# Kernel optimization log

Measured on AMD Instinct MI355X. Metric: run time of the kernel, lower is better.

Reference implementation:

```python
import jax, jax.numpy as jnp
import numpy as np

EPS = 1e-4

def _mlp2(x, W1, b1, W2, b2):
    # Sequential(Linear, ReLU, Linear) -> [*, 1]
    return jax.nn.relu(x @ W1 + b1) @ W2 + b2

def setup_inputs() -> dict:
    N, D = 400, 64
    key = jax.random.key(0)
    ks = jax.random.split(key, 24)
    s = 0.1
    inp = {
        "t": 0,
        "node_edge_embedding": jax.random.normal(ks[0], (N + N * N, D), jnp.float32),
        "node_flow_norm": jax.random.normal(ks[1], (N, D), jnp.float32),
        "A_ne": jax.random.uniform(ks[2], (N, N * N), jnp.float32),
        "node_num": N,
        # alpha_n_dedunce
        "W_alpha": jax.random.normal(ks[3], (D, D), jnp.float32) * s,
        "b_alpha": jnp.zeros((D,), jnp.float32),
        # gamma_e_dedunce
        "W_gamma": jax.random.normal(ks[4], (D, D), jnp.float32) * s,
        "b_gamma": jnp.zeros((D,), jnp.float32),
        # node_to_edge (2D -> D)
        "W_n2e": jax.random.normal(ks[5], (2 * D, D), jnp.float32) * s,
        "b_n2e": jnp.zeros((D,), jnp.float32),
        # edge_to_value: D -> D//2 -> 1
        "W_ev1": jax.random.normal(ks[6], (D, D // 2), jnp.float32) * s,
        "b_ev1": jnp.zeros((D // 2,), jnp.float32),
        "W_ev2": jax.random.normal(ks[7], (D // 2, 1), jnp.float32) * s,
        "b_ev2": jnp.zeros((1,), jnp.float32),
        # f_theta: D -> D//2 -> 1
        "W_ft1": jax.random.normal(ks[8], (D, D // 2), jnp.float32) * s,
        "b_ft1": jnp.zeros((D // 2,), jnp.float32),
        "W_ft2": jax.random.normal(ks[9], (D // 2, 1), jnp.float32) * s,
        "b_ft2": jnp.zeros((1,), jnp.float32),
        # W_3, W_4 (init.normal_ std=0.1)
        "W3": jax.random.normal(ks[10], (D, D), jnp.float32) * s,
        "W4": jax.random.normal(ks[11], (D, D), jnp.float32) * s,
        # edge_to_edge
        "W_e2e": jax.random.normal(ks[12], (D, D), jnp.float32) * s,
        "b_e2e": jnp.zeros((D,), jnp.float32),
        # node_to_edge_2 (2D -> D)
        "W_n2e2": jax.random.normal(ks[13], (2 * D, D), jnp.float32) * s,
        "b_n2e2": jnp.zeros((D,), jnp.float32),
    }
    return inp

def reference(t, node_edge_embedding, node_flow_norm, A_ne, node_num,
              W_alpha, b_alpha, W_gamma, b_gamma, W_n2e, b_n2e,
              W_ev1, b_ev1, W_ev2, b_ev2, W_ft1, b_ft1, W_ft2, b_ft2,
              W3, W4, W_e2e, b_e2e, W_n2e2, b_n2e2):
    N = node_num
    D = node_flow_norm.shape[1]
    node_emb = node_edge_embedding[:N]          # [N, D]
    edge_emb = node_edge_embedding[N:]          # [N*N, D]

    # fully-connected cartesian edge features: edges[i*N+j] = [node_i, node_j]
    edges = jnp.concatenate(
        [jnp.broadcast_to(node_emb[:, None, :], (N, N, D)),
         jnp.broadcast_to(node_emb[None, :, :], (N, N, D))], axis=-1
    ).reshape(N * N, 2 * D)                     # [N*N, 2D]

    h = edges @ W_n2e + b_n2e                   # node_to_edge
    A = jax.nn.relu(_mlp2(h, W_ev1, b_ev1, W_ev2, b_ev2)).reshape(N, N)

    # degree normalization: D_mat A D_mat with D_mat = diag(1/sqrt(clamp(rowsum)))
    d = 1.0 / jnp.sqrt(jnp.maximum(jnp.sum(A, axis=1), EPS))  # [N]
    normalized_A = d[:, None] * A * d[None, :]

    massage_conv = (normalized_A @ node_emb) @ W3
    alpha_n = massage_conv @ W_alpha + b_alpha
    alpha_n = alpha_n / jnp.maximum(jnp.max(jnp.abs(alpha_n)), EPS)

    denominator = _mlp2(node_flow_norm, W_ft1, b_ft1, W_ft2, b_ft2)   # [N,1]
    norm_value = _mlp2(node_emb, W_ft1, b_ft1, W_ft2, b_ft2) / \
        jnp.where(denominator == 0, EPS, denominator)
    node_self_evolve = norm_value * (jax.nn.relu(node_flow_norm - node_emb) @ W4)
    node_self_evolve = alpha_n * node_self_evolve

    gamma_e = jax.nn.softmax(edge_emb @ W_gamma + b_gamma, axis=1)    # [N*N, D]
    edge_indicator = jnp.where(A < 1.0, 0.0, 1.0).reshape(-1, 1)      # [N*N, 1]
    Aggr_edge = A_ne @ (edge_indicator * gamma_e * edge_emb)          # [N, D]
    pred_node = node_self_evolve + Aggr_edge

    edge_self_evolve = edge_emb @ W_e2e + b_e2e
    edge_infonode = edges @ W_n2e2 + b_n2e2
    pred_edge = edge_indicator * (edge_self_evolve + edge_infonode)

    pred_node_edge = jnp.concatenate([pred_node, pred_edge], axis=0)
    return pred_node_edge, edge_indicator
```

## Files before the change

kernel.cpp:

```cpp
#include <hip/hip_runtime.h>

#define NV_N 400
#define NN   160000
#define EPSV 1e-4f
#define IND_BASE ((size_t)160400 * 64)

#define OFF_A    0
#define OFF_P2   160000
#define OFF_Q2   172800
#define OFF_R    185600
#define OFF_S    211200
#define OFF_V4   236800
#define OFF_AR   262400
#define OFF_NV   288000
#define OFF_DV   288400
#define OFF_GMAX 288800
#define OFF_CNT  288832
#define OFF_LIST 289280
#define OFF_WV   449280

__global__ __launch_bounds__(64) void k1_node_pre(
    const float* __restrict__ NEE, const float* __restrict__ NFN,
    const float* __restrict__ W_n2e, const float* __restrict__ b_n2e,
    const float* __restrict__ W_n2e2, const float* __restrict__ b_n2e2,
    const float* __restrict__ W_ev1, const float* __restrict__ b_ev1,
    const float* __restrict__ W4,
    const float* __restrict__ W_ft1, const float* __restrict__ b_ft1,
    const float* __restrict__ W_ft2, const float* __restrict__ b_ft2,
    float* __restrict__ ws)
{
    __shared__ float xne[64], xnf[64], tP[64], tQ[64], hidN[32], hidF[32];
    int i = blockIdx.x, dd = threadIdx.x;
    float x_ne = NEE[i*64+dd];
    float x_nf = NFN[i*64+dd];
    xne[dd] = x_ne; xnf[dd] = x_nf;
    if (i == 0 && dd == 0) ((unsigned*)(ws + OFF_GMAX))[0] = 0u;
    __syncthreads();
    float pv = b_n2e[dd], qv = 0.f, rv = b_n2e2[dd], sv = 0.f, v4 = 0.f;
    for (int k = 0; k < 64; ++k) {
        float xk = xne[k];
        pv += xk * W_n2e[k*64+dd];
        qv += xk * W_n2e[(64+k)*64+dd];
        rv += xk * W_n2e2[k*64+dd];
        sv += xk * W_n2e2[(64+k)*64+dd];
        v4 += fmaxf(xnf[k]-xk, 0.f) * W4[k*64+dd];
    }
    tP[dd] = pv; tQ[dd] = qv;
    ws[OFF_R  + i*64+dd] = rv;
    ws[OFF_S  + i*64+dd] = sv;
    ws[OFF_V4 + i*64+dd] = v4;
    if (dd < 32) {
        float hn = b_ft1[dd], hf = b_ft1[dd];
        for (int k = 0; k < 64; ++k) { hn += xne[k]*W_ft1[k*32+dd]; hf += xnf[k]*W_ft1[k*32+dd]; }
        hidN[dd] = fmaxf(hn, 0.f); hidF[dd] = fmaxf(hf, 0.f);
    }
    __syncthreads();
    if (dd < 32) {
        float p2 = b_ev1[dd], q2 = 0.f;
        for (int c = 0; c < 64; ++c) { p2 += tP[c]*W_ev1[c*32+dd]; q2 += tQ[c]*W_ev1[c*32+dd]; }
        ws[OFF_P2 + i*32+dd] = p2;
        ws[OFF_Q2 + i*32+dd] = q2;
    }
    if (dd == 0) {
        float num = b_ft2[0], den = b_ft2[0];
        for (int c = 0; c < 32; ++c) { num += hidN[c]*W_ft2[c]; den += hidF[c]*W_ft2[c]; }
        float dv = (den == 0.f) ? EPSV : den;
        ws[OFF_NV + i] = num / dv;
    }
}

__global__ __launch_bounds__(256) void k2_row(
    const float* __restrict__ NEE,
    const float* __restrict__ W_ev2, const float* __restrict__ b_ev2,
    const float* __restrict__ W_e2e, const float* __restrict__ b_e2e,
    float* __restrict__ ws, float* __restrict__ out)
{
    __shared__ float p2s[32], wev2[32], red[256];
    __shared__ int rcnt[256];
    __shared__ unsigned char flag[NV_N];
    __shared__ int act[NV_N];
    __shared__ int s_cnt;
    int i = blockIdx.x, t = threadIdx.x;
    if (t < 32) { p2s[t] = ws[OFF_P2 + i*32+t]; wev2[t] = W_ev2[t]; }
    __syncthreads();
    float b2 = b_ev2[0];
    float s = 0.f; int cc = 0;
    for (int j = t; j < NV_N; j += 256) {
        float v = b2;
        #pragma unroll
        for (int c = 0; c < 32; ++c) {
            float h = p2s[c] + ws[OFF_Q2 + j*32+c];
            v += fmaxf(h, 0.f) * wev2[c];
        }
        float a = fmaxf(v, 0.f);
        ws[OFF_A + i*NV_N + j] = a;
        bool f = (a >= 1.0f);
        flag[j] = f ? 1 : 0;
        out[IND_BASE + (size_t)i*NV_N + j] = f ? 1.f : 0.f;
        s += a; cc += f ? 1 : 0;
    }
    red[t] = s; rcnt[t] = cc;
    __syncthreads();
    for (int st = 128; st > 0; st >>= 1) {
        if (t < st) { red[t] += red[t+st]; rcnt[t] += rcnt[t+st]; }
        __syncthreads();
    }
    if (t == 0) {
        ws[OFF_DV + i] = rsqrtf(fmaxf(red[0], EPSV));
        ((int*)ws)[OFF_CNT + i] = rcnt[0];
    }
    if (t < 64) {
        int base = 0;
        for (int ch = 0; ch < 7; ++ch) {
            int j = ch*64 + t;
            bool f = (j < NV_N) && (flag[j] != 0);
            unsigned long long m = __ballot(f);
            if (f) {
                int pre = __popcll(m & ((1ull << t) - 1ull));
                act[base + pre] = j;
            }
            base += __popcll(m);
        }
        if (t == 0) s_cnt = base;
    }
    float4 z4 = make_float4(0.f, 0.f, 0.f, 0.f);
    float4* orow = (float4*)(out + (NV_N + (size_t)i*NV_N) * 64);
    for (int q = t; q < NV_N*64/4; q += 256) orow[q] = z4;
    __syncthreads();
    int cnt = s_cnt, lane = t & 63, w = t >> 6;
    for (int k = w; k < cnt; k += 4) {
        int j = act[k];
        int e = i*NV_N + j;
        float emb = NEE[(size_t)(NV_N + e)*64 + lane];
        float v = b_e2e[lane] + ws[OFF_R + i*64 + lane] + ws[OFF_S + j*64 + lane];
        #pragma unroll
        for (int c = 0; c < 64; ++c) v += __shfl(emb, c) * W_e2e[c*64 + lane];
        out[(size_t)(NV_N + e)*64 + lane] = v;
    }
}

__global__ __launch_bounds__(256) void k3_alpha_compact(
    const float* __restrict__ NEE,
    const float* __restrict__ W3,
    const float* __restrict__ W_alpha, const float* __restrict__ b_alpha,
    const float* __restrict__ W_gamma, const float* __restrict__ b_gamma,
    float* __restrict__ ws, int cap)
{
    __shared__ float part[4][64];
    __shared__ int red[256];
    __shared__ int s_off;
    int i = blockIdx.x, t = threadIdx.x, lane = t & 63, w = t >> 6;
    int os = 0;
    for (int r = t; r < i; r += 256) os += ((const int*)ws)[OFF_CNT + r];
    red[t] = os; __syncthreads();
    for (int st = 128; st > 0; st >>= 1) { if (t < st) red[t] += red[t+st]; __syncthreads(); }
    if (t == 0) s_off = red[0];
    float acc = 0.f;
    for (int j = w*100; j < w*100 + 100; ++j) {
        float coef = ws[OFF_A + i*NV_N + j] * ws[OFF_DV + j];
        acc += coef * NEE[j*64 + lane];
    }
    part[w][lane] = acc;
    __syncthreads();
    if (w == 0) {
        float nm = (part[0][lane] + part[1][lane] + part[2][lane] + part[3][lane]) * ws[OFF_DV + i];
        float mc = 0.f;
        #pragma unroll
        for (int c = 0; c < 64; ++c) mc += __shfl(nm, c) * W3[c*64 + lane];
        float ar = b_alpha[lane];
        #pragma unroll
        for (int c = 0; c < 64; ++c) ar += __shfl(mc, c) * W_alpha[c*64 + lane];
        ws[OFF_AR + i*64 + lane] = ar;
        float mx = fabsf(ar);
        #pragma unroll
        for (int off = 32; off > 0; off >>= 1) mx = fmaxf(mx, __shfl_xor(mx, off));
        if (lane == 0) atomicMax((unsigned*)(ws + OFF_GMAX), __float_as_uint(mx));
    } else if (w == 1) {
        int base = 0;
        for (int ch = 0; ch < 7; ++ch) {
            int j = ch*64 + lane;
            float a = (j < NV_N) ? ws[OFF_A + i*NV_N + j] : 0.f;
            bool f = (a >= 1.0f);
            unsigned long long m = __ballot(f);
            if (f) {
                int pre = __popcll(m & ((1ull << lane) - 1ull));
                int slot = s_off + base + pre;
                if (slot < cap) ((int*)ws)[OFF_LIST + slot] = i*NV_N + j;
            }
            base += __popcll(m);
        }
    }
    __syncthreads();
    int cnt = ((const int*)ws)[OFF_CNT + i];
    for (int k = w; k < cnt; k += 4) {
        int slot = s_off + k;
        if (slot >= cap) break;
        int e = ((const int*)ws)[OFF_LIST + slot];
        float emb = NEE[(size_t)(NV_N + e)*64 + lane];
        float g = b_gamma[lane];
        #pragma unroll
        for (int c = 0; c < 64; ++c) g += __shfl(emb, c) * W_gamma[c*64 + lane];
        float mx = g;
        #pragma unroll
        for (int off = 32; off > 0; off >>= 1) mx = fmaxf(mx, __shfl_xor(mx, off));
        float p = __expf(g - mx);
        float ssum = p;
        #pragma unroll
        for (int off = 32; off > 0; off >>= 1) ssum += __shfl_xor(ssum, off);
        ws[OFF_WV + (size_t)slot*64 + lane] = (p / ssum) * emb;
    }
}

__global__ __launch_bounds__(256) void k4_final(
    const float* __restrict__ A_ne,
    const float* __restrict__ ws, int cap,
    float* __restrict__ out)
{
    __shared__ float part[4][64];
    __shared__ int red[256];
    int i = blockIdx.x, t = threadIdx.x, lane = t & 63, w = t >> 6;
    int os = 0;
    for (int r = t; r < NV_N; r += 256) os += ((const int*)ws)[OFF_CNT + r];
    red[t] = os; __syncthreads();
    for (int st = 128; st > 0; st >>= 1) { if (t < st) red[t] += red[t+st]; __syncthreads(); }
    int nnz = red[0]; if (nnz > cap) nnz = cap;
    float acc = 0.f;
    for (int l = w; l < nnz; l += 4) {
        int e = ((const int*)ws)[OFF_LIST + l];
        float a = A_ne[(size_t)i*NN + e];
        acc += a * ws[OFF_WV + (size_t)l*64 + lane];
    }
    part[w][lane] = acc;
    __syncthreads();
    if (w == 0) {
        float aggr = part[0][lane] + part[1][lane] + part[2][lane] + part[3][lane];
        float amax = fmaxf(__uint_as_float(((const unsigned*)(ws + OFF_GMAX))[0]), EPSV);
        float v = (ws[OFF_AR + i*64 + lane] / amax) * ws[OFF_NV + i] * ws[OFF_V4 + i*64 + lane];
        out[i*64 + lane] = v + aggr;
    }
}

extern "C" void kernel_launch(void* const* d_in, const int* in_sizes, int n_in,
                              void* d_out, int out_size, void* d_ws, size_t ws_size,
                              hipStream_t stream) {
    const float* NEE     = (const float*)d_in[1];
    const float* NFN     = (const float*)d_in[2];
    const float* A_ne    = (const float*)d_in[3];
    const float* W_alpha = (const float*)d_in[5];
    const float* b_alpha = (const float*)d_in[6];
    const float* W_gamma = (const float*)d_in[7];
    const float* b_gamma = (const float*)d_in[8];
    const float* W_n2e   = (const float*)d_in[9];
    const float* b_n2e   = (const float*)d_in[10];
    const float* W_ev1   = (const float*)d_in[11];
    const float* b_ev1   = (const float*)d_in[12];
    const float* W_ev2   = (const float*)d_in[13];
    const float* b_ev2   = (const float*)d_in[14];
    const float* W_ft1   = (const float*)d_in[15];
    const float* b_ft1   = (const float*)d_in[16];
    const float* W_ft2   = (const float*)d_in[17];
    const float* b_ft2   = (const float*)d_in[18];
    const float* W3      = (const float*)d_in[19];
    const float* W4      = (const float*)d_in[20];
    const float* W_e2e   = (const float*)d_in[21];
    const float* b_e2e   = (const float*)d_in[22];
    const float* W_n2e2  = (const float*)d_in[23];
    const float* b_n2e2  = (const float*)d_in[24];
    float* out = (float*)d_out;
    float* ws  = (float*)d_ws;

    long long cap_ll = ((long long)(ws_size / 4) - OFF_WV) / 64;
    int cap = (cap_ll > NN) ? NN : (cap_ll < 0 ? 0 : (int)cap_ll);

    hipLaunchKernelGGL(k1_node_pre, dim3(NV_N), dim3(64), 0, stream,
        NEE, NFN, W_n2e, b_n2e, W_n2e2, b_n2e2, W_ev1, b_ev1, W4,
        W_ft1, b_ft1, W_ft2, b_ft2, ws);
    hipLaunchKernelGGL(k2_row, dim3(NV_N), dim3(256), 0, stream,
        NEE, W_ev2, b_ev2, W_e2e, b_e2e, ws, out);
    hipLaunchKernelGGL(k3_alpha_compact, dim3(NV_N), dim3(256), 0, stream,
        NEE, W3, W_alpha, b_alpha, W_gamma, b_gamma, ws, cap);
    hipLaunchKernelGGL(k4_final, dim3(NV_N), dim3(256), 0, stream,
        A_ne, ws, cap, out);
}
```

Baseline: 44.15 us.

## Move edge-output zero fill into first kernel and stage A_ne gathers in LDS

The zeroing of the large edge output block moves out of the per-row kernel and into the first kernel, which now runs on a 2048-block grid of 256 threads that fills the output with a grid-stride loop alongside the node precompute on the first 400 blocks. The final aggregation kernel now gathers A_ne values for the active-edge list into shared memory in chunks using all threads, then accumulates from LDS, instead of each wave issuing scattered global loads inline. The intent is to spread the roughly 41 MB zero write across more parallelism and to batch the irregular A_ne gathers. In exchange there are extra barriers and a 32 KB LDS buffer, which may reduce occupancy.

```diff
diff --git a/kernel.cpp b/kernel.cpp
--- a/kernel.cpp
+++ b/kernel.cpp
@@ -19,7 +19,7 @@
 #define OFF_LIST 289280
 #define OFF_WV   449280
 
-__global__ __launch_bounds__(64) void k1_node_pre(
+__global__ __launch_bounds__(256) void k0_fill_pre(
     const float* __restrict__ NEE, const float* __restrict__ NFN,
     const float* __restrict__ W_n2e, const float* __restrict__ b_n2e,
     const float* __restrict__ W_n2e2, const float* __restrict__ b_n2e2,
@@ -27,46 +27,55 @@
     const float* __restrict__ W4,
     const float* __restrict__ W_ft1, const float* __restrict__ b_ft1,
     const float* __restrict__ W_ft2, const float* __restrict__ b_ft2,
-    float* __restrict__ ws)
+    float* __restrict__ ws, float* __restrict__ out)
 {
     __shared__ float xne[64], xnf[64], tP[64], tQ[64], hidN[32], hidF[32];
-    int i = blockIdx.x, dd = threadIdx.x;
-    float x_ne = NEE[i*64+dd];
-    float x_nf = NFN[i*64+dd];
-    xne[dd] = x_ne; xnf[dd] = x_nf;
-    if (i == 0 && dd == 0) ((unsigned*)(ws + OFF_GMAX))[0] = 0u;
-    __syncthreads();
-    float pv = b_n2e[dd], qv = 0.f, rv = b_n2e2[dd], sv = 0.f, v4 = 0.f;
-    for (int k = 0; k < 64; ++k) {
-        float xk = xne[k];
-        pv += xk * W_n2e[k*64+dd];
-        qv += xk * W_n2e[(64+k)*64+dd];
-        rv += xk * W_n2e2[k*64+dd];
-        sv += xk * W_n2e2[(64+k)*64+dd];
-        v4 += fmaxf(xnf[k]-xk, 0.f) * W4[k*64+dd];
-    }
-    tP[dd] = pv; tQ[dd] = qv;
-    ws[OFF_R  + i*64+dd] = rv;
-    ws[OFF_S  + i*64+dd] = sv;
-    ws[OFF_V4 + i*64+dd] = v4;
-    if (dd < 32) {
-        float hn = b_ft1[dd], hf = b_ft1[dd];
-        for (int k = 0; k < 64; ++k) { hn += xne[k]*W_ft1[k*32+dd]; hf += xnf[k]*W_ft1[k*32+dd]; }
-        hidN[dd] = fmaxf(hn, 0.f); hidF[dd] = fmaxf(hf, 0.f);
-    }
-    __syncthreads();
-    if (dd < 32) {
-        float p2 = b_ev1[dd], q2 = 0.f;
-        for (int c = 0; c < 64; ++c) { p2 += tP[c]*W_ev1[c*32+dd]; q2 += tQ[c]*W_ev1[c*32+dd]; }
-        ws[OFF_P2 + i*32+dd] = p2;
-        ws[OFF_Q2 + i*32+dd] = q2;
-    }
-    if (dd == 0) {
-        float num = b_ft2[0], den = b_ft2[0];
-        for (int c = 0; c < 32; ++c) { num += hidN[c]*W_ft2[c]; den += hidF[c]*W_ft2[c]; }
-        float dv = (den == 0.f) ? EPSV : den;
-        ws[OFF_NV + i] = num / dv;
-    }
+    int b = blockIdx.x, t = threadIdx.x;
+    if (b < NV_N) {
+        int i = b;
+        if (t < 64) { xne[t] = NEE[i*64+t]; xnf[t] = NFN[i*64+t]; }
+        if (b == 0 && t == 0) ((unsigned*)(ws + OFF_GMAX))[0] = 0u;
+        __syncthreads();
+        if (t < 64) {
+            int dd = t;
+            float pv = b_n2e[dd], qv = 0.f, rv = b_n2e2[dd], sv = 0.f, v4 = 0.f;
+            for (int k = 0; k < 64; ++k) {
+                float xk = xne[k];
+                pv += xk * W_n2e[k*64+dd];
+                qv += xk * W_n2e[(64+k)*64+dd];
+                rv += xk * W_n2e2[k*64+dd];
+                sv += xk * W_n2e2[(64+k)*64+dd];
+                v4 += fmaxf(xnf[k]-xk, 0.f) * W4[k*64+dd];
+            }
+            tP[dd] = pv; tQ[dd] = qv;
+            ws[OFF_R  + i*64+dd] = rv;
+            ws[OFF_S  + i*64+dd] = sv;
+            ws[OFF_V4 + i*64+dd] = v4;
+        } else if (t >= 64 && t < 96) {
+            int dd = t - 64;
+            float hn = b_ft1[dd], hf = b_ft1[dd];
+            for (int k = 0; k < 64; ++k) { hn += xne[k]*W_ft1[k*32+dd]; hf += xnf[k]*W_ft1[k*32+dd]; }
+            hidN[dd] = fmaxf(hn, 0.f); hidF[dd] = fmaxf(hf, 0.f);
+        }
+        __syncthreads();
+        if (t < 32) {
+            float p2 = b_ev1[t], q2 = 0.f;
+            for (int c = 0; c < 64; ++c) { p2 += tP[c]*W_ev1[c*32+t]; q2 += tQ[c]*W_ev1[c*32+t]; }
+            ws[OFF_P2 + i*32+t] = p2;
+            ws[OFF_Q2 + i*32+t] = q2;
+        }
+        if (t == 96) {
+            float num = b_ft2[0], den = b_ft2[0];
+            for (int c = 0; c < 32; ++c) { num += hidN[c]*W_ft2[c]; den += hidF[c]*W_ft2[c]; }
+            float dv = (den == 0.f) ? EPSV : den;
+            ws[OFF_NV + i] = num / dv;
+        }
+    }
+    const float4 z4 = make_float4(0.f, 0.f, 0.f, 0.f);
+    float4* dst = (float4*)(out + (size_t)NV_N * 64);
+    size_t nq = (size_t)NN * 16;
+    for (size_t q = (size_t)b*256 + t; q < nq; q += (size_t)gridDim.x * 256)
+        dst[q] = z4;
 }
 
 __global__ __launch_bounds__(256) void k2_row(
@@ -123,9 +132,6 @@
         }
         if (t == 0) s_cnt = base;
     }
-    float4 z4 = make_float4(0.f, 0.f, 0.f, 0.f);
-    float4* orow = (float4*)(out + (NV_N + (size_t)i*NV_N) * 64);
-    for (int q = t; q < NV_N*64/4; q += 256) orow[q] = z4;
     __syncthreads();
     int cnt = s_cnt, lane = t & 63, w = t >> 6;
     for (int k = w; k < cnt; k += 4) {
@@ -211,11 +217,13 @@
     }
 }
 
+#define LCHUNK 8192
 __global__ __launch_bounds__(256) void k4_final(
     const float* __restrict__ A_ne,
     const float* __restrict__ ws, int cap,
     float* __restrict__ out)
 {
+    __shared__ float av[LCHUNK];
     __shared__ float part[4][64];
     __shared__ int red[256];
     int i = blockIdx.x, t = threadIdx.x, lane = t & 63, w = t >> 6;
@@ -224,11 +232,18 @@
     red[t] = os; __syncthreads();
     for (int st = 128; st > 0; st >>= 1) { if (t < st) red[t] += red[t+st]; __syncthreads(); }
     int nnz = red[0]; if (nnz > cap) nnz = cap;
+    const float* Arow = A_ne + (size_t)i * NN;
     float acc = 0.f;
-    for (int l = w; l < nnz; l += 4) {
-        int e = ((const int*)ws)[OFF_LIST + l];
-        float a = A_ne[(size_t)i*NN + e];
-        acc += a * ws[OFF_WV + (size_t)l*64 + lane];
+    for (int base = 0; base < nnz; base += LCHUNK) {
+        int m = nnz - base; if (m > LCHUNK) m = LCHUNK;
+        __syncthreads();
+        for (int l = t; l < m; l += 256) {
+            int e = ((const int*)ws)[OFF_LIST + base + l];
+            av[l] = Arow[e];
+        }
+        __syncthreads();
+        for (int l = w; l < m; l += 4)
+            acc = fmaf(av[l], ws[OFF_WV + (size_t)(base + l)*64 + lane], acc);
     }
     part[w][lane] = acc;
     __syncthreads();
@@ -272,9 +287,9 @@
     long long cap_ll = ((long long)(ws_size / 4) - OFF_WV) / 64;
     int cap = (cap_ll > NN) ? NN : (cap_ll < 0 ? 0 : (int)cap_ll);
 
-    hipLaunchKernelGGL(k1_node_pre, dim3(NV_N), dim3(64), 0, stream,
+    hipLaunchKernelGGL(k0_fill_pre, dim3(2048), dim3(256), 0, stream,
         NEE, NFN, W_n2e, b_n2e, W_n2e2, b_n2e2, W_ev1, b_ev1, W4,
-        W_ft1, b_ft1, W_ft2, b_ft2, ws);
+        W_ft1, b_ft1, W_ft2, b_ft2, ws, out);
     hipLaunchKernelGGL(k2_row, dim3(NV_N), dim3(256), 0, stream,
         NEE, W_ev2, b_ev2, W_e2e, b_e2e, ws, out);
     hipLaunchKernelGGL(k3_alpha_compact, dim3(NV_N), dim3(256), 0, stream,
```

Result: faster. 41.91 us (-5.1%).
